# Kernel tuning notes

Hardware: AMD Instinct MI355X
Metric: run time of the kernel (lower is better)

## Reference

```python
import jax, jax.numpy as jnp
import numpy as np

N_NODES = 100000
N_EDGES = 1200000
D_IN = 64
D_HID = 64


def _gcn_layer(h_in, W, b, src, dst, norm, n_nodes):
    # h_in: [N, d_in]; W: [d_in, d_out]; norm: [E_total] symmetric deg norm
    h = h_in @ W                                  # [N, d_out]
    msg = h[src] * norm[:, None]                  # gather + scale, [E_total, d_out]
    agg = jax.ops.segment_sum(msg, dst, num_segments=n_nodes)  # scatter-add
    return agg + b


def _prelu(x, a):
    # per-channel PReLU: a broadcasts over nodes
    return jnp.where(x >= 0, x, a * x)


def setup_inputs() -> dict:
    key = jax.random.key(0)
    ks = jax.random.split(key, 8)
    x = jax.random.normal(ks[0], (N_NODES, D_IN), dtype=jnp.float32)
    edge_index = jax.random.randint(ks[1], (2, N_EDGES), 0, N_NODES, dtype=jnp.int64)
    # Glorot-ish weights, PyG GCNConv defaults: weight + bias; PReLU init slope 0.25
    W1 = jax.random.normal(ks[2], (D_IN, D_HID), dtype=jnp.float32) / np.sqrt(D_IN)
    b1 = jnp.zeros((D_HID,), dtype=jnp.float32)
    a1 = jnp.full((D_HID,), 0.25, dtype=jnp.float32)
    W2 = jax.random.normal(ks[3], (D_HID, D_HID), dtype=jnp.float32) / np.sqrt(D_HID)
    b2 = jnp.zeros((D_HID,), dtype=jnp.float32)
    a2 = jnp.full((D_HID,), 0.25, dtype=jnp.float32)
    return {"x": x, "edge_index": edge_index, "W1": W1, "b1": b1, "a1": a1,
            "W2": W2, "b2": b2, "a2": a2}


def reference(x, edge_index, W1, b1, a1, W2, b2, a2):
    n = x.shape[0]
    # add self-loops (GCNConv default add_self_loops=True)
    loops = jnp.arange(n, dtype=edge_index.dtype)
    src = jnp.concatenate([edge_index[0], loops])
    dst = jnp.concatenate([edge_index[1], loops])
    # symmetric normalization: deg computed on destination with unit edge weights
    deg = jax.ops.segment_sum(jnp.ones_like(src, dtype=x.dtype), dst, num_segments=n)
    dinv = jnp.where(deg > 0, jax.lax.rsqrt(deg), 0.0)
    norm = dinv[src] * dinv[dst]                  # [E + N]

    h = _gcn_layer(x, W1, b1, src, dst, norm, n)
    h = _prelu(h, a1)
    h = _gcn_layer(h, W2, b2, src, dst, norm, n)
    h = _prelu(h, a2)
    return h
```

## Files before the change

### kernel.cpp

```cpp
#include <hip/hip_runtime.h>
#include <hip/hip_bf16.h>
#include <hip/hip_fp16.h>

#define D 64
#define NB 256
#define BSHIFT 8
#define NBK 512
#define SUBS 8
#define SCAP 1024
#define CHUNK 8192
#define AGN 32
#define BFSTRIDE 16

typedef _Float16 f16x8 __attribute__((ext_vector_type(8)));
typedef float    f32x4 __attribute__((ext_vector_type(4)));


__global__ void __launch_bounds__(256, 4)
k_bin_gemm(const int* __restrict__ src, const int* __restrict__ dst,
           unsigned* __restrict__ records, int* __restrict__ bucket_fill,
           int E, int nbin,
           const float* __restrict__ X, const float* __restrict__ W,
           __half* __restrict__ H, int n, int ntiles, int gemmb) {
    __shared__ int cnt[NBK];
    __shared__ int gbase[NBK];
    const int t = threadIdx.x;

    if ((int)blockIdx.x < nbin) {
        const int slot = blockIdx.x & (SUBS - 1);
        cnt[t] = 0; cnt[t + 256] = 0;
        __syncthreads();

        const int base_e = blockIdx.x * CHUNK;
        unsigned rec[32];
        unsigned br[32];
#pragma unroll
        for (int i = 0; i < 8; ++i) {
            const int e0 = base_e + i * 1024 + t * 4;
            if (e0 + 3 < E) {
                int4 s4 = *reinterpret_cast<const int4*>(src + e0);
                int4 d4 = *reinterpret_cast<const int4*>(dst + e0);
                int ss[4] = {s4.x, s4.y, s4.z, s4.w};
                int dd[4] = {d4.x, d4.y, d4.z, d4.w};
#pragma unroll
                for (int j = 0; j < 4; ++j) {
                    int bk = dd[j] >> BSHIFT;
                    rec[i * 4 + j] = ((unsigned)ss[j] << BSHIFT) | (unsigned)(dd[j] & (NB - 1));
                    int rank = atomicAdd(&cnt[bk], 1);
                    br[i * 4 + j] = ((unsigned)bk << 16) | (unsigned)rank;
                }
            } else {
#pragma unroll
                for (int j = 0; j < 4; ++j) {
                    int e = e0 + j;
                    if (e < E) {
                        int s = src[e], d = dst[e];
                        int bk = d >> BSHIFT;
                        rec[i * 4 + j] = ((unsigned)s << BSHIFT) | (unsigned)(d & (NB - 1));
                        int rank = atomicAdd(&cnt[bk], 1);
                        br[i * 4 + j] = ((unsigned)bk << 16) | (unsigned)rank;
                    } else {
                        br[i * 4 + j] = 0xFFFFFFFFu;
                    }
                }
            }
        }
        __syncthreads();
#pragma unroll
        for (int rep = 0; rep < NBK / 256; ++rep) {
            int bk = t + rep * 256;
            if (cnt[bk] > 0)
                gbase[bk] = atomicAdd(&bucket_fill[(bk * SUBS + slot) * BFSTRIDE], cnt[bk]);
        }
        __syncthreads();
#pragma unroll
        for (int i = 0; i < 32; ++i) {
            if (br[i] != 0xFFFFFFFFu) {
                int bk = br[i] >> 16;
                int idx = gbase[bk] + (int)(br[i] & 0xFFFF);
                if (idx < SCAP)
                    records[((size_t)bk * SUBS + slot) * SCAP + idx] = rec[i];
            }
        }
    } else {
        const int lane = t & 63;
        const int wv   = t >> 6;
        const int r16  = lane & 15;
        const int g4   = lane >> 4;

        f16x8 Bh[4][2], Bl[4][2];
#pragma unroll
        for (int ct = 0; ct < 4; ++ct)
#pragma unroll
            for (int kt = 0; kt < 2; ++kt)
#pragma unroll
                for (int j = 0; j < 8; ++j) {
                    float w = W[(kt * 32 + g4 * 8 + j) * D + ct * 16 + r16];
                    _Float16 h = (_Float16)w;
                    Bh[ct][kt][j] = h;
                    Bl[ct][kt][j] = (_Float16)(w - (float)h);
                }

        const int gw = (blockIdx.x - nbin) * 4 + wv;
        for (int tile = gw; tile < ntiles; tile += gemmb * 4) {
            const int nb16 = tile * 16;
            int row = nb16 + r16;
            if (row > n - 1) row = n - 1;
            const float* xp = X + (size_t)row * D + g4 * 8;
            float4 x0 = *reinterpret_cast<const float4*>(xp);
            float4 x1 = *reinterpret_cast<const float4*>(xp + 4);
            float4 x2 = *reinterpret_cast<const float4*>(xp + 32);
            float4 x3 = *reinterpret_cast<const float4*>(xp + 36);
            float xs[16] = {x0.x, x0.y, x0.z, x0.w, x1.x, x1.y, x1.z, x1.w,
                            x2.x, x2.y, x2.z, x2.w, x3.x, x3.y, x3.z, x3.w};
            f16x8 Ah[2], Al[2];
#pragma unroll
            for (int kt = 0; kt < 2; ++kt)
#pragma unroll
                for (int j = 0; j < 8; ++j) {
                    float v = xs[kt * 8 + j];
                    _Float16 h = (_Float16)v;
                    Ah[kt][j] = h;
                    Al[kt][j] = (_Float16)(v - (float)h);
                }

            f32x4 acc[4];
#pragma unroll
            for (int ct = 0; ct < 4; ++ct)
                acc[ct] = (f32x4){0.f, 0.f, 0.f, 0.f};
#pragma unroll
            for (int ct = 0; ct < 4; ++ct) {
#pragma unroll
                for (int kt = 0; kt < 2; ++kt) {
                    acc[ct] = __builtin_amdgcn_mfma_f32_16x16x32_f16(Ah[kt], Bh[ct][kt], acc[ct], 0, 0, 0);
                    acc[ct] = __builtin_amdgcn_mfma_f32_16x16x32_f16(Al[kt], Bh[ct][kt], acc[ct], 0, 0, 0);
                    acc[ct] = __builtin_amdgcn_mfma_f32_16x16x32_f16(Ah[kt], Bl[ct][kt], acc[ct], 0, 0, 0);
                }
            }
#pragma unroll
            for (int ct = 0; ct < 4; ++ct)
#pragma unroll
                for (int r = 0; r < 4; ++r) {
                    int node = nb16 + g4 * 4 + r;
                    if (node < n)
                        H[(size_t)node * D + ct * 16 + r16] = __float2half_rn(acc[ct][r]);
                }
        }
    }
}


__global__ void k_csr(const unsigned* __restrict__ records,
                      const int* __restrict__ bucket_fill,
                      int* __restrict__ edge_base,
                      int* __restrict__ rowbeg, int* __restrict__ rowcnt,
                      float* __restrict__ dinv,
                      int* __restrict__ csr_src, int n) {
    __shared__ int cnt[NB];
    __shared__ int excl[NB];
    __shared__ int wsum[4];
    __shared__ int sbase;
    __shared__ int stage[SUBS * SCAP];

    const int t = threadIdx.x;
    const int b = blockIdx.x;
    const int lane = t & 63;

    int subcnt[SUBS];
    int cnt_e = 0;
#pragma unroll
    for (int s = 0; s < SUBS; ++s) {
        subcnt[s] = bucket_fill[(b * SUBS + s) * BFSTRIDE];
        cnt_e += subcnt[s];
    }

    cnt[t] = 0;
    __syncthreads();
#pragma unroll
    for (int s = 0; s < SUBS; ++s) {
        const size_t so = ((size_t)b * SUBS + s) * SCAP;
        for (int i = t; i < subcnt[s]; i += 256)
            atomicAdd(&cnt[records[so + i] & (NB - 1)], 1);
    }
    __syncthreads();

    const int c0 = cnt[t];
    int v = c0;
#pragma unroll
    for (int off = 1; off < 64; off <<= 1) {
        int u = __shfl_up(v, off, 64);
        if (lane >= off) v += u;
    }
    if (lane == 63) wsum[t >> 6] = v;
    if (t == 0) sbase = atomicAdd(edge_base, cnt_e);
    __syncthreads();
    int pre = 0;
#pragma unroll
    for (int w = 0; w < 4; ++w)
        if (w < (t >> 6)) pre += wsum[w];
    const int ex = v + pre - c0;
    excl[t] = ex;
    const int base = sbase;
    {
        int node = b * NB + t;
        if (node < n) {
            rowbeg[node] = base + ex;
            rowcnt[node] = c0;
            dinv[node]   = rsqrtf((float)(c0 + 1));
        }
    }
    cnt[t] = 0;
    __syncthreads();

#pragma unroll
    for (int s = 0; s < SUBS; ++s) {
        const size_t so = ((size_t)b * SUBS + s) * SCAP;
        for (int i = t; i < subcnt[s]; i += 256) {
            unsigned r = records[so + i];
            int d8 = r & (NB - 1);
            int rank = atomicAdd(&cnt[d8], 1);
            stage[excl[d8] + rank] = (int)(r >> BSHIFT);
        }
    }
    __syncthreads();

    for (int i = t; i < cnt_e; i += 256)
        csr_src[base + i] = stage[i];
}

__device__ __forceinline__ void edge_accum(const __half* __restrict__ Hn,
                                           const int* __restrict__ csr_src,
                                           int beg, int end, int part, float acc[8]) {
    int idx[8];
#pragma unroll
    for (int j = 0; j < 8; ++j)
        idx[j] = (beg + j < end) ? csr_src[beg + j] : 0;
    int k = beg;
    while (k < end) {
        int s[8];
        float w[8];
#pragma unroll
        for (int j = 0; j < 8; ++j) {
            s[j] = idx[j];
            w[j] = (k + j < end) ? 1.f : 0.f;
        }
        int kn = k + 8;
#pragma unroll
        for (int j = 0; j < 8; ++j)
            idx[j] = (kn + j < end) ? csr_src[kn + j] : 0;
        uint4 g[8];
#pragma unroll
        for (int j = 0; j < 8; ++j)
            g[j] = *reinterpret_cast<const uint4*>(Hn + (size_t)s[j] * D + part);
#pragma unroll
        for (int j = 0; j < 8; ++j) {
            const __half2* p = reinterpret_cast<const __half2*>(&g[j]);
#pragma unroll
            for (int i = 0; i < 4; ++i) {
                float2 f = __half22float2(p[i]);
                acc[2 * i + 0] += w[j] * f.x;
                acc[2 * i + 1] += w[j] * f.y;
            }
        }
        k = kn;
    }
}

__device__ __forceinline__ void edge_accum_sc(const __half* __restrict__ Hn,
                                              const int* __restrict__ csr_src,
                                              const float* __restrict__ dinv,
                                              int beg, int end, int part, float acc[8]) {
    int idx[8];
    float dv[8];
#pragma unroll
    for (int j = 0; j < 8; ++j)
        idx[j] = (beg + j < end) ? csr_src[beg + j] : 0;
#pragma unroll
    for (int j = 0; j < 8; ++j)
        dv[j] = dinv[idx[j]];
    int k = beg;
    while (k < end) {
        int s[8];
        float w[8];
#pragma unroll
        for (int j = 0; j < 8; ++j) {
            s[j] = idx[j];
            w[j] = (k + j < end) ? dv[j] : 0.f;
        }
        int kn = k + 8;
#pragma unroll
        for (int j = 0; j < 8; ++j)
            idx[j] = (kn + j < end) ? csr_src[kn + j] : 0;
#pragma unroll
        for (int j = 0; j < 8; ++j)
            dv[j] = dinv[idx[j]];
        uint4 g[8];
#pragma unroll
        for (int j = 0; j < 8; ++j)
            g[j] = *reinterpret_cast<const uint4*>(Hn + (size_t)s[j] * D + part);
#pragma unroll
        for (int j = 0; j < 8; ++j) {
            const __half2* p = reinterpret_cast<const __half2*>(&g[j]);
#pragma unroll
            for (int i = 0; i < 4; ++i) {
                float2 f = __half22float2(p[i]);
                acc[2 * i + 0] += w[j] * f.x;
                acc[2 * i + 1] += w[j] * f.y;
            }
        }
        k = kn;
    }
}


__global__ void __launch_bounds__(256, 5)
k_agg_gemm(const __half* __restrict__ Hn1,
           const int* __restrict__ rowbeg,
           const int* __restrict__ rowcnt,
           const int* __restrict__ csr_src,
           const float* __restrict__ dinv,
           const float* __restrict__ b1, const float* __restrict__ a1,
           const float* __restrict__ W2,
           __half* __restrict__ Hn2, int n) {
    __shared__ _Float16 W2h[D * D];
    __shared__ _Float16 W2s[D * D];
    __shared__ float Yl[AGN][68];

    const int t = threadIdx.x;

#pragma unroll
    for (int q = 0; q < 4; ++q) {
        float4 wq = *reinterpret_cast<const float4*>(W2 + t * 16 + q * 4);
        float ws[4] = {wq.x, wq.y, wq.z, wq.w};
#pragma unroll
        for (int m = 0; m < 4; ++m) {
            int widx = t * 16 + q * 4 + m;
            int k   = widx >> 6;
            int col = widx & 63;
            int li  = (((k >> 5) * 4 + ((k >> 3) & 3)) * 64 + col) * 8 + (k & 7);
            _Float16 h = (_Float16)ws[m];
            W2h[li] = h;
            W2s[li] = (_Float16)(ws[m] - (float)h);
        }
    }

    const int nl   = t >> 3;
    const int part = (t & 7) * 8;
    const int node = blockIdx.x * AGN + nl;

    if (node < n) {
        float di = dinv[node];
        float acc[8];
        {
            uint4 g = *reinterpret_cast<const uint4*>(Hn1 + (size_t)node * D + part);
            const __half2* p = reinterpret_cast<const __half2*>(&g);
#pragma unroll
            for (int i = 0; i < 4; ++i) {
                float2 f = __half22float2(p[i]);
                acc[2 * i + 0] = f.x * di;
                acc[2 * i + 1] = f.y * di;
            }
        }
        const int beg = rowbeg[node];
        edge_accum_sc(Hn1, csr_src, dinv, beg, beg + rowcnt[node], part, acc);

        const float4 b0 = *reinterpret_cast<const float4*>(b1 + part);
        const float4 b4 = *reinterpret_cast<const float4*>(b1 + part + 4);
        const float4 a0 = *reinterpret_cast<const float4*>(a1 + part);
        const float4 a4 = *reinterpret_cast<const float4*>(a1 + part + 4);
        float y0 = acc[0] * di + b0.x, y1 = acc[1] * di + b0.y;
        float y2 = acc[2] * di + b0.z, y3 = acc[3] * di + b0.w;
        float y4 = acc[4] * di + b4.x, y5 = acc[5] * di + b4.y;
        float y6 = acc[6] * di + b4.z, y7 = acc[7] * di + b4.w;
        Yl[nl][part + 0] = (y0 >= 0.f) ? y0 : a0.x * y0;
        Yl[nl][part + 1] = (y1 >= 0.f) ? y1 : a0.y * y1;
        Yl[nl][part + 2] = (y2 >= 0.f) ? y2 : a0.z * y2;
        Yl[nl][part + 3] = (y3 >= 0.f) ? y3 : a0.w * y3;
        Yl[nl][part + 4] = (y4 >= 0.f) ? y4 : a4.x * y4;
        Yl[nl][part + 5] = (y5 >= 0.f) ? y5 : a4.y * y5;
        Yl[nl][part + 6] = (y6 >= 0.f) ? y6 : a4.z * y6;
        Yl[nl][part + 7] = (y7 >= 0.f) ? y7 : a4.w * y7;
        if ((t & 7) == 0) Yl[nl][64] = di;
    }
    __syncthreads();

    {
        const int lane = t & 63;
        const int wvq  = t >> 6;
        const int r16  = lane & 15;
        const int g4   = lane >> 4;
        const int rt   = wvq >> 1;
        const int cp   = wvq & 1;

        f32x4 acc2[2];
        acc2[0] = (f32x4){0.f, 0.f, 0.f, 0.f};
        acc2[1] = (f32x4){0.f, 0.f, 0.f, 0.f};
#pragma unroll
        for (int kt = 0; kt < 2; ++kt) {
            const float* yp = &Yl[rt * 16 + r16][kt * 32 + g4 * 8];
            f16x8 Ah, Al;
#pragma unroll
            for (int j = 0; j < 8; ++j) {
                float v = yp[j];
                _Float16 h = (_Float16)v;
                Ah[j] = h;
                Al[j] = (_Float16)(v - (float)h);
            }
#pragma unroll
            for (int ci = 0; ci < 2; ++ci) {
                int li = ((kt * 4 + g4) * 64 + (cp * 2 + ci) * 16 + r16) * 8;
                f16x8 Bh = *reinterpret_cast<const f16x8*>(&W2h[li]);
                f16x8 Bl = *reinterpret_cast<const f16x8*>(&W2s[li]);
                acc2[ci] = __builtin_amdgcn_mfma_f32_16x16x32_f16(Ah, Bh, acc2[ci], 0, 0, 0);
                acc2[ci] = __builtin_amdgcn_mfma_f32_16x16x32_f16(Al, Bh, acc2[ci], 0, 0, 0);
                acc2[ci] = __builtin_amdgcn_mfma_f32_16x16x32_f16(Ah, Bl, acc2[ci], 0, 0, 0);
            }
        }
#pragma unroll
        for (int ci = 0; ci < 2; ++ci)
#pragma unroll
            for (int r = 0; r < 4; ++r) {
                int row = rt * 16 + g4 * 4 + r;
                int nd  = blockIdx.x * AGN + row;
                if (nd < n) {
                    float dr = Yl[row][64];
                    Hn2[(size_t)nd * D + (cp * 2 + ci) * 16 + r16] =
                        __float2half_rn(acc2[ci][r] * dr);
                }
            }
    }
}


__global__ void k_aggregate(const __half* __restrict__ Hn,
                            const int* __restrict__ rowbeg,
                            const int* __restrict__ rowcnt,
                            const int* __restrict__ csr_src,
                            const float* __restrict__ dinv,
                            const float* __restrict__ b, const float* __restrict__ a,
                            float* __restrict__ out, int n) {
    int t = blockIdx.x * blockDim.x + threadIdx.x;
    int node = t >> 3;
    if (node >= n) return;
    int part = (t & 7) * 8;

    float di = dinv[node];
    float acc[8];
    {
        uint4 g = *reinterpret_cast<const uint4*>(Hn + (size_t)node * D + part);
        const __half2* p = reinterpret_cast<const __half2*>(&g);
#pragma unroll
        for (int i = 0; i < 4; ++i) {
            float2 f = __half22float2(p[i]);
            acc[2 * i + 0] = f.x;
            acc[2 * i + 1] = f.y;
        }
    }
    const int beg = rowbeg[node];
    edge_accum(Hn, csr_src, beg, beg + rowcnt[node], part, acc);

    const float4 b0 = *reinterpret_cast<const float4*>(b + part);
    const float4 b4 = *reinterpret_cast<const float4*>(b + part + 4);
    const float4 a0 = *reinterpret_cast<const float4*>(a + part);
    const float4 a4 = *reinterpret_cast<const float4*>(a + part + 4);
    float4 r0, r1;
    r0.x = acc[0] * di + b0.x; r0.y = acc[1] * di + b0.y;
    r0.z = acc[2] * di + b0.z; r0.w = acc[3] * di + b0.w;
    r1.x = acc[4] * di + b4.x; r1.y = acc[5] * di + b4.y;
    r1.z = acc[6] * di + b4.z; r1.w = acc[7] * di + b4.w;
    r0.x = (r0.x >= 0.f) ? r0.x : a0.x * r0.x;
    r0.y = (r0.y >= 0.f) ? r0.y : a0.y * r0.y;
    r0.z = (r0.z >= 0.f) ? r0.z : a0.z * r0.z;
    r0.w = (r0.w >= 0.f) ? r0.w : a0.w * r0.w;
    r1.x = (r1.x >= 0.f) ? r1.x : a4.x * r1.x;
    r1.y = (r1.y >= 0.f) ? r1.y : a4.y * r1.y;
    r1.z = (r1.z >= 0.f) ? r1.z : a4.z * r1.z;
    r1.w = (r1.w >= 0.f) ? r1.w : a4.w * r1.w;
    float* o = out + (size_t)node * D + part;
    *reinterpret_cast<float4*>(o) = r0;
    *reinterpret_cast<float4*>(o + 4) = r1;
}

extern "C" void kernel_launch(void* const* d_in, const int* in_sizes, int n_in,
                              void* d_out, int out_size, void* d_ws, size_t ws_size,
                              hipStream_t stream) {
    const float* x  = (const float*)d_in[0];
    const int*   ei = (const int*)  d_in[1];
    const float* W1 = (const float*)d_in[2];
    const float* b1 = (const float*)d_in[3];
    const float* a1 = (const float*)d_in[4];
    const float* W2 = (const float*)d_in[5];
    const float* b2 = (const float*)d_in[6];
    const float* a2 = (const float*)d_in[7];
    float* out = (float*)d_out;

    const int n   = in_sizes[0] / D;
    const int E   = in_sizes[1] / 2;
    const int n64 = n * D;

    const int* src = ei;
    const int* dst = ei + E;

    const int nbuckets = (n + NB - 1) >> BSHIFT;

    int*      bucket_fill = (int*)d_ws;
    int*      edge_base   = bucket_fill + 60000;
    unsigned* records     = (unsigned*)(bucket_fill + 4096 * BFSTRIDE);
    int*      rowbeg      = (int*)(records + (size_t)nbuckets * SUBS * SCAP);
    int*      rowcnt      = rowbeg + ((n + 256) & ~255);
    float*    dinv        = (float*)(rowcnt + ((n + 256) & ~255));
    int*      csr_src     = (int*)(dinv + ((n + 256) & ~255));
    __half*   Hn1         = (__half*)(csr_src + ((E + 255) & ~255));
    __half*   Hn2         = Hn1 + (((size_t)n64 + 256) & ~(size_t)255);

    const int B = 256;
    const int nbin   = (E + CHUNK - 1) / CHUNK;
    const int gemmb  = 877;
    const int ntiles = (n + 15) / 16;

    hipMemsetAsync(bucket_fill, 0, 4096 * BFSTRIDE * sizeof(int), stream);

    k_bin_gemm<<<nbin + gemmb, B, 0, stream>>>(src, dst, records, bucket_fill, E, nbin,
                                               x, W1, Hn1, n, ntiles, gemmb);
    k_csr<<<nbuckets, B, 0, stream>>>(records, bucket_fill, edge_base,
                                      rowbeg, rowcnt, dinv, csr_src, n);
    k_agg_gemm<<<(n + AGN - 1) / AGN, B, 0, stream>>>(Hn1, rowbeg, rowcnt, csr_src, dinv,
                                                      b1, a1, W2, Hn2, n);
    k_aggregate<<<(n * 8 + B - 1) / B, B, 0, stream>>>(Hn2, rowbeg, rowcnt, csr_src, dinv,
                                                       b2, a2, out, n);
}
```

Before: 175.9 us.

## Stage W1 in LDS, prefetch two GEMM tiles per wave, widen CSR blocks

The GEMM path of the fused bin/GEMM kernel now splits W1 into hi/lo fp16 halves once per block in shared memory, instead of holding them in registers per lane. Each wave now handles exactly two tiles, loading both X rows before computing either, so the global-load latency overlaps. The grid size is retuned so two tiles per wave cover the node count. The CSR build kernel moves to 512-thread blocks to add parallelism to its record counting and scatter loops. In exchange, the fixed two-tile loop silently drops tiles if the node count grows past what the grid covers. The extra 16KB of shared memory also applies to the binning blocks.

```diff
diff --git a/kernel.cpp b/kernel.cpp
--- a/kernel.cpp
+++ b/kernel.cpp
@@ -24,6 +24,8 @@
            __half* __restrict__ H, int n, int ntiles, int gemmb) {
     __shared__ int cnt[NBK];
     __shared__ int gbase[NBK];
+    __shared__ _Float16 W1h[D * D];
+    __shared__ _Float16 W1s[D * D];
     const int t = threadIdx.x;
 
     if ((int)blockIdx.x < nbin) {
@@ -88,31 +90,33 @@
         const int r16  = lane & 15;
         const int g4   = lane >> 4;
 
-        f16x8 Bh[4][2], Bl[4][2];
-#pragma unroll
-        for (int ct = 0; ct < 4; ++ct)
-#pragma unroll
-            for (int kt = 0; kt < 2; ++kt)
-#pragma unroll
-                for (int j = 0; j < 8; ++j) {
-                    float w = W[(kt * 32 + g4 * 8 + j) * D + ct * 16 + r16];
-                    _Float16 h = (_Float16)w;
-                    Bh[ct][kt][j] = h;
-                    Bl[ct][kt][j] = (_Float16)(w - (float)h);
-                }
+#pragma unroll
+        for (int q = 0; q < 4; ++q) {
+            float4 wq = *reinterpret_cast<const float4*>(W + t * 16 + q * 4);
+            float ws[4] = {wq.x, wq.y, wq.z, wq.w};
+#pragma unroll
+            for (int m = 0; m < 4; ++m) {
+                int widx = t * 16 + q * 4 + m;
+                int k   = widx >> 6;
+                int col = widx & 63;
+                int li  = (((k >> 5) * 4 + ((k >> 3) & 3)) * 64 + col) * 8 + (k & 7);
+                _Float16 h = (_Float16)ws[m];
+                W1h[li] = h;
+                W1s[li] = (_Float16)(ws[m] - (float)h);
+            }
+        }
+        __syncthreads();
 
         const int gw = (blockIdx.x - nbin) * 4 + wv;
-        for (int tile = gw; tile < ntiles; tile += gemmb * 4) {
-            const int nb16 = tile * 16;
-            int row = nb16 + r16;
-            if (row > n - 1) row = n - 1;
-            const float* xp = X + (size_t)row * D + g4 * 8;
-            float4 x0 = *reinterpret_cast<const float4*>(xp);
-            float4 x1 = *reinterpret_cast<const float4*>(xp + 4);
-            float4 x2 = *reinterpret_cast<const float4*>(xp + 32);
-            float4 x3 = *reinterpret_cast<const float4*>(xp + 36);
-            float xs[16] = {x0.x, x0.y, x0.z, x0.w, x1.x, x1.y, x1.z, x1.w,
-                            x2.x, x2.y, x2.z, x2.w, x3.x, x3.y, x3.z, x3.w};
+        const int stride = gemmb * 4;
+        const int t0 = gw;
+        const int t1 = gw + stride;
+
+        auto run_tile = [&](int tile, const float4* xv) {
+            float xs[16] = {xv[0].x, xv[0].y, xv[0].z, xv[0].w,
+                            xv[1].x, xv[1].y, xv[1].z, xv[1].w,
+                            xv[2].x, xv[2].y, xv[2].z, xv[2].w,
+                            xv[3].x, xv[3].y, xv[3].z, xv[3].w};
             f16x8 Ah[2], Al[2];
 #pragma unroll
             for (int kt = 0; kt < 2; ++kt)
@@ -123,7 +127,6 @@
                     Ah[kt][j] = h;
                     Al[kt][j] = (_Float16)(v - (float)h);
                 }
-
             f32x4 acc[4];
 #pragma unroll
             for (int ct = 0; ct < 4; ++ct)
@@ -132,11 +135,15 @@
             for (int ct = 0; ct < 4; ++ct) {
 #pragma unroll
                 for (int kt = 0; kt < 2; ++kt) {
-                    acc[ct] = __builtin_amdgcn_mfma_f32_16x16x32_f16(Ah[kt], Bh[ct][kt], acc[ct], 0, 0, 0);
-                    acc[ct] = __builtin_amdgcn_mfma_f32_16x16x32_f16(Al[kt], Bh[ct][kt], acc[ct], 0, 0, 0);
-                    acc[ct] = __builtin_amdgcn_mfma_f32_16x16x32_f16(Ah[kt], Bl[ct][kt], acc[ct], 0, 0, 0);
+                    int li = ((kt * 4 + g4) * 64 + ct * 16 + r16) * 8;
+                    f16x8 Bh = *reinterpret_cast<const f16x8*>(&W1h[li]);
+                    f16x8 Bl = *reinterpret_cast<const f16x8*>(&W1s[li]);
+                    acc[ct] = __builtin_amdgcn_mfma_f32_16x16x32_f16(Ah[kt], Bh, acc[ct], 0, 0, 0);
+                    acc[ct] = __builtin_amdgcn_mfma_f32_16x16x32_f16(Al[kt], Bh, acc[ct], 0, 0, 0);
+                    acc[ct] = __builtin_amdgcn_mfma_f32_16x16x32_f16(Ah[kt], Bl, acc[ct], 0, 0, 0);
                 }
             }
+            const int nb16 = tile * 16;
 #pragma unroll
             for (int ct = 0; ct < 4; ++ct)
 #pragma unroll
@@ -145,17 +152,40 @@
                     if (node < n)
                         H[(size_t)node * D + ct * 16 + r16] = __float2half_rn(acc[ct][r]);
                 }
-        }
-    }
-}
-
-
-__global__ void k_csr(const unsigned* __restrict__ records,
-                      const int* __restrict__ bucket_fill,
-                      int* __restrict__ edge_base,
-                      int* __restrict__ rowbeg, int* __restrict__ rowcnt,
-                      float* __restrict__ dinv,
-                      int* __restrict__ csr_src, int n) {
+        };
+
+        float4 xa[4], xb[4];
+        if (t0 < ntiles) {
+            int row = t0 * 16 + r16;
+            if (row > n - 1) row = n - 1;
+            const float* xp = X + (size_t)row * D + g4 * 8;
+            xa[0] = *reinterpret_cast<const float4*>(xp);
+            xa[1] = *reinterpret_cast<const float4*>(xp + 4);
+            xa[2] = *reinterpret_cast<const float4*>(xp + 32);
+            xa[3] = *reinterpret_cast<const float4*>(xp + 36);
+        }
+        if (t1 < ntiles) {
+            int row = t1 * 16 + r16;
+            if (row > n - 1) row = n - 1;
+            const float* xp = X + (size_t)row * D + g4 * 8;
+            xb[0] = *reinterpret_cast<const float4*>(xp);
+            xb[1] = *reinterpret_cast<const float4*>(xp + 4);
+            xb[2] = *reinterpret_cast<const float4*>(xp + 32);
+            xb[3] = *reinterpret_cast<const float4*>(xp + 36);
+        }
+        if (t0 < ntiles) run_tile(t0, xa);
+        if (t1 < ntiles) run_tile(t1, xb);
+    }
+}
+
+
+__global__ void __launch_bounds__(512)
+k_csr(const unsigned* __restrict__ records,
+      const int* __restrict__ bucket_fill,
+      int* __restrict__ edge_base,
+      int* __restrict__ rowbeg, int* __restrict__ rowcnt,
+      float* __restrict__ dinv,
+      int* __restrict__ csr_src, int n) {
     __shared__ int cnt[NB];
     __shared__ int excl[NB];
     __shared__ int wsum[4];
@@ -174,48 +204,50 @@
         cnt_e += subcnt[s];
     }
 
-    cnt[t] = 0;
+    if (t < NB) cnt[t] = 0;
     __syncthreads();
 #pragma unroll
     for (int s = 0; s < SUBS; ++s) {
         const size_t so = ((size_t)b * SUBS + s) * SCAP;
-        for (int i = t; i < subcnt[s]; i += 256)
+        for (int i = t; i < subcnt[s]; i += 512)
             atomicAdd(&cnt[records[so + i] & (NB - 1)], 1);
     }
     __syncthreads();
 
-    const int c0 = cnt[t];
-    int v = c0;
-#pragma unroll
-    for (int off = 1; off < 64; off <<= 1) {
-        int u = __shfl_up(v, off, 64);
-        if (lane >= off) v += u;
-    }
-    if (lane == 63) wsum[t >> 6] = v;
+    int c0 = 0, v = 0;
+    if (t < NB) {
+        c0 = cnt[t];
+        v = c0;
+#pragma unroll
+        for (int off = 1; off < 64; off <<= 1) {
+            int u = __shfl_up(v, off, 64);
+            if (lane >= off) v += u;
+        }
+        if (lane == 63) wsum[t >> 6] = v;
+    }
     if (t == 0) sbase = atomicAdd(edge_base, cnt_e);
     __syncthreads();
-    int pre = 0;
-#pragma unroll
-    for (int w = 0; w < 4; ++w)
-        if (w < (t >> 6)) pre += wsum[w];
-    const int ex = v + pre - c0;
-    excl[t] = ex;
-    const int base = sbase;
-    {
+    if (t < NB) {
+        int pre = 0;
+#pragma unroll
+        for (int w = 0; w < 4; ++w)
+            if (w < (t >> 6)) pre += wsum[w];
+        const int ex = v + pre - c0;
+        excl[t] = ex;
         int node = b * NB + t;
         if (node < n) {
-            rowbeg[node] = base + ex;
+            rowbeg[node] = sbase + ex;
             rowcnt[node] = c0;
             dinv[node]   = rsqrtf((float)(c0 + 1));
         }
-    }
-    cnt[t] = 0;
+        cnt[t] = 0;
+    }
     __syncthreads();
 
 #pragma unroll
     for (int s = 0; s < SUBS; ++s) {
         const size_t so = ((size_t)b * SUBS + s) * SCAP;
-        for (int i = t; i < subcnt[s]; i += 256) {
+        for (int i = t; i < subcnt[s]; i += 512) {
             unsigned r = records[so + i];
             int d8 = r & (NB - 1);
             int rank = atomicAdd(&cnt[d8], 1);
@@ -224,7 +256,8 @@
     }
     __syncthreads();
 
-    for (int i = t; i < cnt_e; i += 256)
+    const int base = sbase;
+    for (int i = t; i < cnt_e; i += 512)
         csr_src[base + i] = stage[i];
 }
 
@@ -515,15 +548,15 @@
 
     const int B = 256;
     const int nbin   = (E + CHUNK - 1) / CHUNK;
-    const int gemmb  = 877;
     const int ntiles = (n + 15) / 16;
+    const int gemmb  = 782;
 
     hipMemsetAsync(bucket_fill, 0, 4096 * BFSTRIDE * sizeof(int), stream);
 
     k_bin_gemm<<<nbin + gemmb, B, 0, stream>>>(src, dst, records, bucket_fill, E, nbin,
                                                x, W1, Hn1, n, ntiles, gemmb);
-    k_csr<<<nbuckets, B, 0, stream>>>(records, bucket_fill, edge_base,
-                                      rowbeg, rowcnt, dinv, csr_src, n);
+    k_csr<<<nbuckets, 512, 0, stream>>>(records, bucket_fill, edge_base,
+                                        rowbeg, rowcnt, dinv, csr_src, n);
     k_agg_gemm<<<(n + AGN - 1) / AGN, B, 0, stream>>>(Hn1, rowbeg, rowcnt, csr_src, dinv,
                                                       b1, a1, W2, Hn2, n);
     k_aggregate<<<(n * 8 + B - 1) / B, B, 0, stream>>>(Hn2, rowbeg, rowcnt, csr_src, dinv,
```

New measurement: 174.7 us. Within noise of the previous version (-0.6%).
